# Kernel optimization log

Hardware: AMD Instinct MI355X
Metric: run time of the kernel (lower is better)

## Reference

```python
import jax, jax.numpy as jnp
import numpy as np


def setup_inputs() -> dict:
    key = jax.random.key(0)
    x = jax.random.normal(key, (64, 1048576), dtype=jnp.float32)
    return {"x": x}


def reference(x) -> jnp.ndarray:
    x_flat = x.reshape(-1)
    n = x_flat.shape[0]
    k = 1

    # Standard top-k (k=1): lax.top_k returns the value and its index.
    _, idx_std = jax.lax.top_k(x_flat, k)  # [k]

    # stable_topk: flip, stable descending sort, map index back.
    reversed_x = x_flat[::-1]
    # Stable ascending argsort of -x == stable descending argsort of x
    # (negation preserves tie groups; stable sort preserves their order).
    order = jnp.argsort(-reversed_x)  # jnp.argsort is stable by default
    top_k_reversed_indices = order[:k]
    idx_stb = (n - 1) - top_k_reversed_indices  # reversed_indices gather

    return jnp.any(idx_std != idx_stb)
```

## Files before the change

### kernel.cpp

```cpp
#include <hip/hip_runtime.h>
#include <math.h>


#define NB 2048
#define NT 256

struct Trip { float v; int imin; int imax; };

__device__ __forceinline__ void upd(float x, int idx, float& v, int& imin, int& imax) {
    if (x > v)      { v = x; imin = idx; imax = idx; }
    else if (x == v){ if (idx < imin) imin = idx; if (idx > imax) imax = idx; }
}

__device__ __forceinline__ void merge(float bv, int bmn, int bmx,
                                      float& v, int& imin, int& imax) {
    if (bv > v)       { v = bv; imin = bmn; imax = bmx; }
    else if (bv == v) { if (bmn < imin) imin = bmn; if (bmx > imax) imax = bmx; }
}

__global__ __launch_bounds__(NT) void argmax_part(const float4* __restrict__ x,
                                                  Trip* __restrict__ part, int n4) {
    const int tid = blockIdx.x * NT + threadIdx.x;
    const int stride = NB * NT;
    float v = -INFINITY; int imin = 0x7fffffff, imax = -1;
    for (int i = tid; i < n4; i += stride) {
        float4 f = x[i];
        int b = i << 2;
        upd(f.x, b,     v, imin, imax);
        upd(f.y, b + 1, v, imin, imax);
        upd(f.z, b + 2, v, imin, imax);
        upd(f.w, b + 3, v, imin, imax);
    }

    __shared__ float sv[NT];
    __shared__ int   smn[NT], smx[NT];
    const int t = threadIdx.x;
    sv[t] = v; smn[t] = imin; smx[t] = imax;
    __syncthreads();
    for (int s = NT / 2; s > 0; s >>= 1) {
        if (t < s) {
            float av = sv[t]; int amn = smn[t], amx = smx[t];
            merge(sv[t + s], smn[t + s], smx[t + s], av, amn, amx);
            sv[t] = av; smn[t] = amn; smx[t] = amx;
        }
        __syncthreads();
    }
    if (t == 0) { part[blockIdx.x].v = sv[0]; part[blockIdx.x].imin = smn[0]; part[blockIdx.x].imax = smx[0]; }
}

__global__ __launch_bounds__(NT) void argmax_final(const Trip* __restrict__ part,
                                                   const float* __restrict__ x,
                                                   int n4, int n,
                                                   int* __restrict__ out) {
    const int t = threadIdx.x;
    float v = -INFINITY; int imin = 0x7fffffff, imax = -1;
    for (int i = t; i < NB; i += NT) {
        Trip p = part[i];
        merge(p.v, p.imin, p.imax, v, imin, imax);
    }
    for (int i = n4 * 4 + t; i < n; i += NT) upd(x[i], i, v, imin, imax);

    __shared__ float sv[NT];
    __shared__ int   smn[NT], smx[NT];
    sv[t] = v; smn[t] = imin; smx[t] = imax;
    __syncthreads();
    for (int s = NT / 2; s > 0; s >>= 1) {
        if (t < s) {
            float av = sv[t]; int amn = smn[t], amx = smx[t];
            merge(sv[t + s], smn[t + s], smx[t + s], av, amn, amx);
            sv[t] = av; smn[t] = amn; smx[t] = amx;
        }
        __syncthreads();
    }
    if (t == 0) out[0] = (smn[0] != smx[0]) ? 1 : 0;
}

extern "C" void kernel_launch(void* const* d_in, const int* in_sizes, int n_in,
                              void* d_out, int out_size, void* d_ws, size_t ws_size,
                              hipStream_t stream) {
    const float* x = (const float*)d_in[0];
    const int n  = in_sizes[0];
    const int n4 = n >> 2;
    Trip* part = (Trip*)d_ws;

    argmax_part <<<NB, NT, 0, stream>>>((const float4*)x, part, n4);
    argmax_final<<<1,  NT, 0, stream>>>(part, x, n4, n, (int*)d_out);
}
```

Baseline: 49.35 us.

## Fuse partial and final argmax into one kernel using 64-bit atomics and ticket

Replaces the two-kernel reduction (per-block partials, then a single-block final pass) with one kernel. Each block packs its max value and min/max index into 64-bit keys and combines them with atomicMax, and the last block to take a ticket writes the result. This removes the second launch and the partial-buffer round trip. In exchange it adds a memset launch each call, a few contended global atomics, and threadfence ordering that the result depends on.

```diff
diff --git a/kernel.cpp b/kernel.cpp
--- a/kernel.cpp
+++ b/kernel.cpp
@@ -5,7 +5,7 @@
 #define NB 2048
 #define NT 256
 
-struct Trip { float v; int imin; int imax; };
+struct Ctl { unsigned long long kmin; unsigned long long kmax; unsigned int ticket; };
 
 __device__ __forceinline__ void upd(float x, int idx, float& v, int& imin, int& imax) {
     if (x > v)      { v = x; imin = idx; imax = idx; }
@@ -18,8 +18,15 @@
     else if (bv == v) { if (bmn < imin) imin = bmn; if (bmx > imax) imax = bmx; }
 }
 
-__global__ __launch_bounds__(NT) void argmax_part(const float4* __restrict__ x,
-                                                  Trip* __restrict__ part, int n4) {
+__device__ __forceinline__ unsigned int fmap(float f) {
+    unsigned int u = __float_as_uint(f);
+    return (u & 0x80000000u) ? ~u : (u | 0x80000000u);
+}
+
+__global__ __launch_bounds__(NT) void argmax_fused(const float4* __restrict__ x,
+                                                   Ctl* __restrict__ ctl,
+                                                   int n4, int n,
+                                                   int* __restrict__ out) {
     const int tid = blockIdx.x * NT + threadIdx.x;
     const int stride = NB * NT;
     float v = -INFINITY; int imin = 0x7fffffff, imax = -1;
@@ -30,6 +37,10 @@
         upd(f.y, b + 1, v, imin, imax);
         upd(f.z, b + 2, v, imin, imax);
         upd(f.w, b + 3, v, imin, imax);
+    }
+    if (blockIdx.x == 0) {
+        const float* xs = (const float*)x;
+        for (int i = n4 * 4 + threadIdx.x; i < n; i += NT) upd(xs[i], i, v, imin, imax);
     }
 
     __shared__ float sv[NT];
@@ -45,34 +56,22 @@
         }
         __syncthreads();
     }
-    if (t == 0) { part[blockIdx.x].v = sv[0]; part[blockIdx.x].imin = smn[0]; part[blockIdx.x].imax = smx[0]; }
-}
 
-__global__ __launch_bounds__(NT) void argmax_final(const Trip* __restrict__ part,
-                                                   const float* __restrict__ x,
-                                                   int n4, int n,
-                                                   int* __restrict__ out) {
-    const int t = threadIdx.x;
-    float v = -INFINITY; int imin = 0x7fffffff, imax = -1;
-    for (int i = t; i < NB; i += NT) {
-        Trip p = part[i];
-        merge(p.v, p.imin, p.imax, v, imin, imax);
+    if (t == 0) {
+        unsigned long long mv = (unsigned long long)fmap(sv[0]) << 32;
+        atomicMax(&ctl->kmin, mv | (unsigned int)(~smn[0]));
+        atomicMax(&ctl->kmax, mv | (unsigned int)( smx[0]));
+        __threadfence();
+        unsigned int old = atomicAdd(&ctl->ticket, 1u);
+        if (old == NB - 1) {
+            __threadfence();
+            unsigned long long kmin = atomicMax(&ctl->kmin, 0ULL);
+            unsigned long long kmax = atomicMax(&ctl->kmax, 0ULL);
+            int gimin = (int)(~(unsigned int)kmin);
+            int gimax = (int)( (unsigned int)kmax);
+            out[0] = (gimin != gimax) ? 1 : 0;
+        }
     }
-    for (int i = n4 * 4 + t; i < n; i += NT) upd(x[i], i, v, imin, imax);
-
-    __shared__ float sv[NT];
-    __shared__ int   smn[NT], smx[NT];
-    sv[t] = v; smn[t] = imin; smx[t] = imax;
-    __syncthreads();
-    for (int s = NT / 2; s > 0; s >>= 1) {
-        if (t < s) {
-            float av = sv[t]; int amn = smn[t], amx = smx[t];
-            merge(sv[t + s], smn[t + s], smx[t + s], av, amn, amx);
-            sv[t] = av; smn[t] = amn; smx[t] = amx;
-        }
-        __syncthreads();
-    }
-    if (t == 0) out[0] = (smn[0] != smx[0]) ? 1 : 0;
 }
 
 extern "C" void kernel_launch(void* const* d_in, const int* in_sizes, int n_in,
@@ -81,8 +80,8 @@
     const float* x = (const float*)d_in[0];
     const int n  = in_sizes[0];
     const int n4 = n >> 2;
-    Trip* part = (Trip*)d_ws;
+    Ctl* ctl = (Ctl*)d_ws;
 
-    argmax_part <<<NB, NT, 0, stream>>>((const float4*)x, part, n4);
-    argmax_final<<<1,  NT, 0, stream>>>(part, x, n4, n, (int*)d_out);
+    (void)hipMemsetAsync(d_ws, 0, sizeof(Ctl), stream);
+    argmax_fused<<<NB, NT, 0, stream>>>((const float4*)x, ctl, n4, n, (int*)d_out);
 }
```

Result: slower. 121.5 us (+146.2%).
